# Performance work log

Hardware: AMD Instinct MI355X
Metric: run time of the kernel (lower is better)

The kernel has to match this reference:

```python
import jax, jax.numpy as jnp
import numpy as np

B, T, N = 16, 1024, 512

def setup_inputs() -> dict:
    key = jax.random.key(0)
    ks = jax.random.split(key, 6)
    scale = 1.0 / np.sqrt(N)
    x = jax.random.normal(ks[0], (B, T, N), dtype=jnp.float32)
    Wq = jax.random.normal(ks[1], (N, N), dtype=jnp.float32) * scale
    Wk = jax.random.normal(ks[2], (N, N), dtype=jnp.float32) * scale
    Wv = jax.random.normal(ks[3], (N, N), dtype=jnp.float32) * scale
    Wp = jax.random.normal(ks[4], (N, N), dtype=jnp.float32) * scale
    bp = jnp.zeros((N,), dtype=jnp.float32)
    return {"x": x, "Wq": Wq, "Wk": Wk, "Wv": Wv, "Wp": Wp, "bp": bp}

def reference(x, Wq, Wk, Wv, Wp, bp):
    # x: [B, T, N]; conv1d(k=1) over node channels == 'oi,bit->bot' on x^T [B,N,T]
    xt = jnp.swapaxes(x, -1, -2)                     # [B, N, T]
    q = jnp.einsum('oi,bit->bot', Wq, xt)            # [B, N, T]
    k = jnp.einsum('oi,bit->bot', Wk, xt)
    v = jnp.einsum('oi,bit->bot', Wv, xt)
    n = x.shape[-1]
    attn = jnp.einsum('bnt,bmt->bnm', q, k) * (n ** -0.5)  # [B, N, N]
    attn = jax.nn.softmax(attn, axis=-1)
    px = jnp.einsum('bnm,bmt->bnt', attn, v)         # [B, N, T]
    px = jnp.swapaxes(px, -1, -2)                    # [B, T, N]
    out = jnp.einsum('btn,on->bto', px, Wp) + bp     # Linear(N,N)
    return out
```

## Files before the change

### kernel.cpp

```cpp
#include <hip/hip_runtime.h>
#include <stdint.h>

#define BB 16
#define TT 1024
#define NN 512

typedef unsigned short u16;
typedef __bf16 bf16_t;
typedef bf16_t bf16x8 __attribute__((ext_vector_type(8)));
typedef float f32x4 __attribute__((ext_vector_type(4)));

struct alignas(8) U16x4 { u16 x, y, z, w; };
struct alignas(16) F32x4 { float x, y, z, w; };

__device__ __forceinline__ u16 f2bf(float f) {
    union { float f; uint32_t u; } v; v.f = f;
    uint32_t r = v.u + 0x7fffu + ((v.u >> 16) & 1u);
    return (u16)(r >> 16);
}

__device__ __forceinline__ void gload_lds16(const void* g, void* l) {
    __builtin_amdgcn_global_load_lds(
        (const __attribute__((address_space(1))) void*)g,
        (__attribute__((address_space(3))) void*)l, 16, 0, 0);
}

__device__ __forceinline__ void xcd_swizzle(int gx, int gy, int& bx, int& by) {
    const int nwg  = gx * gy;
    const int orig = by * gx + bx;
    const int q = nwg >> 3, r = nwg & 7;
    const int xcd = orig & 7, loc = orig >> 3;
    const int swz = (xcd < r ? xcd * (q + 1) : r * (q + 1) + (xcd - r) * q) + loc;
    bx = swz % gx;
    by = swz / gx;
}

__global__ __launch_bounds__(256)
void cvt_f32_bf16(const float* __restrict__ in, u16* __restrict__ out, int n4) {
    int i = blockIdx.x * blockDim.x + threadIdx.x;
    int stride = gridDim.x * blockDim.x;
    for (int c = i; c < n4; c += stride) {
        F32x4 f = ((const F32x4*)in)[c];
        U16x4 u;
        u.x = f2bf(f.x); u.y = f2bf(f.y); u.z = f2bf(f.z); u.w = f2bf(f.w);
        ((U16x4*)out)[c] = u;
    }
}

__global__ __launch_bounds__(256)
void cvt_weights(const float* __restrict__ Wq, const float* __restrict__ Wk,
                 const float* __restrict__ Wv, const float* __restrict__ Wp,
                 u16* __restrict__ out) {
    const int c = blockIdx.x * 256 + threadIdx.x;
    const int w = c >> 16;
    const int idx = c & 65535;
    const float* src = (w == 0) ? Wq : (w == 1) ? Wk : (w == 2) ? Wv : Wp;
    F32x4 f = ((const F32x4*)src)[idx];
    U16x4 u;
    u.x = f2bf(f.x); u.y = f2bf(f.y); u.z = f2bf(f.z); u.w = f2bf(f.w);
    ((U16x4*)out)[c] = u;
}

template<int MODE, int SPLITK>
__global__ __launch_bounds__(256)
void gemm_nt(const u16* __restrict__ Ag, const u16* __restrict__ Bg,
             void* __restrict__ Cg, const float* __restrict__ bias,
             int M, int Nc, int K, int lda, int ldb,
             long sA, long sB, long sC)
{
    int zb = blockIdx.z, kof = 0;
    if (SPLITK) { kof = (zb >> 4) * K; zb &= 15; }
    const u16* A  = Ag + (long)zb * sA + kof;
    const u16* Bt = Bg + (long)zb * sB + kof;

    __shared__ u16 As[8192];
    __shared__ u16 Bs[8192];

    int bx = blockIdx.x, by = blockIdx.y;
    xcd_swizzle(gridDim.x, gridDim.y, bx, by);

    const int tid  = threadIdx.x;
    const int wave = tid >> 6;
    const int lane = tid & 63;
    const int arow0 = by * 128;
    const int brow0 = bx * 128;
    const int wr = (wave >> 1) * 64;
    const int wc = (wave & 1) * 64;

    f32x4 zero = {0.f, 0.f, 0.f, 0.f};
    f32x4 acc[4][4];
#pragma unroll
    for (int i = 0; i < 4; i++)
#pragma unroll
        for (int j = 0; j < 4; j++) acc[i][j] = zero;

    const int kTiles = K >> 6;
    for (int kt = 0; kt < kTiles; ++kt) {
#pragma unroll
        for (int it = 0; it < 4; ++it) {
            const int off  = it * 4096 + wave * 1024 + lane * 16;
            const int row  = off >> 7;
            const int kb   = off & 127;
            const int gcol = kb ^ ((row & 7) << 4);
            gload_lds16((const char*)A  + ((long)(arow0 + row) * lda + kt * 64) * 2 + gcol,
                        (char*)As + it * 4096 + wave * 1024);
            gload_lds16((const char*)Bt + ((long)(brow0 + row) * ldb + kt * 64) * 2 + gcol,
                        (char*)Bs + it * 4096 + wave * 1024);
        }
        __syncthreads();

#pragma unroll
        for (int kk = 0; kk < 2; ++kk) {
            bf16x8 av[4], bv[4];
            const int kbyte = kk * 64 + ((lane >> 4) << 4);
#pragma unroll
            for (int m = 0; m < 4; m++) {
                const int row = wr + m * 16 + (lane & 15);
                av[m] = *(const bf16x8*)((const char*)As + row * 128 + (kbyte ^ ((row & 7) << 4)));
            }
#pragma unroll
            for (int n = 0; n < 4; n++) {
                const int row = wc + n * 16 + (lane & 15);
                bv[n] = *(const bf16x8*)((const char*)Bs + row * 128 + (kbyte ^ ((row & 7) << 4)));
            }
#pragma unroll
            for (int m = 0; m < 4; m++)
#pragma unroll
                for (int n = 0; n < 4; n++)
                    acc[m][n] = __builtin_amdgcn_mfma_f32_16x16x32_bf16(av[m], bv[n], acc[m][n], 0, 0, 0);
        }
        __syncthreads();
    }

    const int r0 = (lane >> 4) << 2;
    const int cl = lane & 15;
#pragma unroll
    for (int m = 0; m < 4; m++) {
        const long gm = (long)arow0 + wr + m * 16 + r0;
#pragma unroll
        for (int n = 0; n < 4; n++) {
            const long gn = (long)brow0 + wc + n * 16 + cl;
            if (MODE == 0) {
                u16* O = (u16*)Cg + blockIdx.z * sC;
#pragma unroll
                for (int r = 0; r < 4; r++)
                    O[(gm + r) * Nc + gn] = f2bf(acc[m][n][r]);
            } else if (MODE == 4) {
                const long b = gm >> 10;
                const long t = gm & 1023;
                if (gn < 1024) {
                    u16* O = (u16*)Cg + (gn >> 9) * ((long)BB * NN * TT);
                    const long col = gn & 511;
                    U16x4 u;
                    u.x = f2bf(acc[m][n][0]); u.y = f2bf(acc[m][n][1]);
                    u.z = f2bf(acc[m][n][2]); u.w = f2bf(acc[m][n][3]);
                    *(U16x4*)(O + (b * 512 + col) * 1024 + t) = u;
                } else {
                    u16* V = (u16*)Cg + 2L * BB * NN * TT;
                    const int vc = (int)gn - 1024;
#pragma unroll
                    for (int r = 0; r < 4; r++)
                        V[(gm + r) * NN + vc] = f2bf(acc[m][n][r]);
                }
            } else {
                float* O = (float*)Cg + blockIdx.z * sC;
                const float bb = (MODE == 3) ? bias[gn] : 0.f;
#pragma unroll
                for (int r = 0; r < 4; r++)
                    O[(gm + r) * Nc + gn] = acc[m][n][r] + bb;
            }
        }
    }
}

__global__ __launch_bounds__(256)
void softmax_rows(float* __restrict__ S0, const float* __restrict__ S1)
{
    const long r = blockIdx.x;
    float* row0 = S0 + r * 512;
    const float* row1 = S1 + r * 512;
    const int t = threadIdx.x;
    const int lane = t & 63, wave = t >> 6;
    const float scale = 0.04419417382415922f;

    float a = (row0[t]       + row1[t])       * scale;
    float b = (row0[t + 256] + row1[t + 256]) * scale;

    float m = fmaxf(a, b);
#pragma unroll
    for (int o = 32; o; o >>= 1) m = fmaxf(m, __shfl_xor(m, o, 64));

    __shared__ float red[8];
    if (lane == 0) red[wave] = m;
    __syncthreads();
    m = fmaxf(fmaxf(red[0], red[1]), fmaxf(red[2], red[3]));

    float e0 = __expf(a - m), e1 = __expf(b - m);
    float s = e0 + e1;
#pragma unroll
    for (int o = 32; o; o >>= 1) s += __shfl_xor(s, o, 64);
    if (lane == 0) red[wave + 4] = s;
    __syncthreads();
    s = red[4] + red[5] + red[6] + red[7];
    const float inv = 1.f / s;

    u16* P = (u16*)row0;
    P[t]       = f2bf(e0 * inv);
    P[t + 256] = f2bf(e1 * inv);
}

extern "C" void kernel_launch(void* const* d_in, const int* in_sizes, int n_in,
                              void* d_out, int out_size, void* d_ws, size_t ws_size,
                              hipStream_t stream)
{
    (void)in_sizes; (void)n_in; (void)out_size; (void)ws_size;
    const float* x  = (const float*)d_in[0];
    const float* Wq = (const float*)d_in[1];
    const float* Wk = (const float*)d_in[2];
    const float* Wv = (const float*)d_in[3];
    const float* Wp = (const float*)d_in[4];
    const float* bp = (const float*)d_in[5];
    float* out = (float*)d_out;

    char* ws = (char*)d_ws;
    size_t o = 0;
    auto alloc = [&](size_t bytes) {
        char* p = ws + o;
        o = (o + bytes + 255) & ~(size_t)255;
        return p;
    };
    u16* xb  = (u16*)alloc((size_t)BB * TT * NN * 2);
    u16* wb  = (u16*)alloc((size_t)4 * NN * NN * 2);
    u16* qkv = (u16*)alloc((size_t)3 * BB * NN * TT * 2);
    float* S = (float*)alloc((size_t)2 * BB * NN * NN * 4);
    u16* px  = xb;

    const u16* qb  = qkv;
    const u16* kbp = qkv + (size_t)BB * NN * TT;
    const u16* vb  = qkv + (size_t)2 * BB * NN * TT;
    const u16* wpb = wb + (size_t)3 * NN * NN;
    float* S1 = S + (size_t)BB * NN * NN;

    cvt_f32_bf16<<<dim3(2048), dim3(256), 0, stream>>>(x, xb, (BB * TT * NN) / 4);
    cvt_weights<<<dim3(1024), dim3(256), 0, stream>>>(Wq, Wk, Wv, Wp, wb);

    const dim3 blk(256);

    const dim3 gq(12, 128, 1);
    gemm_nt<4, 0><<<gq, blk, 0, stream>>>(xb, wb, qkv, nullptr,
                                          BB * TT, 1536, NN, NN, NN, 0, 0, 0);

    const dim3 g2(NN / 128, NN / 128, 2 * BB);
    gemm_nt<2, 1><<<g2, blk, 0, stream>>>(qb, kbp, S, nullptr, NN, NN, TT / 2, TT, TT,
                                          (long)NN * TT, (long)NN * TT, (long)NN * NN);

    softmax_rows<<<dim3(BB * NN), dim3(256), 0, stream>>>(S, S1);

    const dim3 g3(NN / 128, TT / 128, BB);
    gemm_nt<0, 0><<<g3, blk, 0, stream>>>(vb, (const u16*)S, px, nullptr, TT, NN, NN, NN, 1024,
                                          (long)TT * NN, (long)NN * 1024, (long)TT * NN);

    const dim3 g1(NN / 128, (BB * TT) / 128, 1);
    gemm_nt<3, 0><<<g1, blk, 0, stream>>>(px, wpb, out, bp, BB * TT, NN, NN, NN, NN, 0, 0, 0);
}
```

Before: 189.9 us.

## Double-buffer GEMM LDS tiles with BK=32 and merge conversion kernels

Rewrites the GEMM main loop to use two 32-wide K tiles in LDS. The next tile is prefetched with global_load_lds while MFMAs run on the current one, using manual vmcnt waits and raw s_barrier in place of __syncthreads. The LDS swizzle is adapted to the 64-byte row layout. It also fuses the x and weight fp32-to-bf16 conversion kernels into one launch with a flat grid. The smaller K tile doubles the barrier count per K, and the hand-written waitcnt logic carries correctness risk.

```diff
diff --git a/kernel.cpp b/kernel.cpp
--- a/kernel.cpp
+++ b/kernel.cpp
@@ -36,29 +36,29 @@
 }
 
 __global__ __launch_bounds__(256)
-void cvt_f32_bf16(const float* __restrict__ in, u16* __restrict__ out, int n4) {
-    int i = blockIdx.x * blockDim.x + threadIdx.x;
-    int stride = gridDim.x * blockDim.x;
-    for (int c = i; c < n4; c += stride) {
-        F32x4 f = ((const F32x4*)in)[c];
-        U16x4 u;
-        u.x = f2bf(f.x); u.y = f2bf(f.y); u.z = f2bf(f.z); u.w = f2bf(f.w);
-        ((U16x4*)out)[c] = u;
+void cvt_all(const float* __restrict__ x,
+             const float* __restrict__ Wq, const float* __restrict__ Wk,
+             const float* __restrict__ Wv, const float* __restrict__ Wp,
+             u16* __restrict__ xb, u16* __restrict__ wb) {
+    int c = blockIdx.x * 256 + threadIdx.x;
+    const float* src;
+    u16* dst;
+    int idx;
+    if (c < 2097152) {
+        src = x; dst = xb; idx = c;
+    } else {
+        c -= 2097152;
+        const int w = c >> 16;
+        idx = c & 65535;
+        src = (w == 0) ? Wq : (w == 1) ? Wk : (w == 2) ? Wv : Wp;
+        dst = wb + (w << 18);
+        idx += 0;
+        dst = wb; idx = (w << 16) + (c & 65535);
     }
-}
-
-__global__ __launch_bounds__(256)
-void cvt_weights(const float* __restrict__ Wq, const float* __restrict__ Wk,
-                 const float* __restrict__ Wv, const float* __restrict__ Wp,
-                 u16* __restrict__ out) {
-    const int c = blockIdx.x * 256 + threadIdx.x;
-    const int w = c >> 16;
-    const int idx = c & 65535;
-    const float* src = (w == 0) ? Wq : (w == 1) ? Wk : (w == 2) ? Wv : Wp;
-    F32x4 f = ((const F32x4*)src)[idx];
+    F32x4 f = ((const F32x4*)src)[ (src == x) ? idx : (idx & 65535) ];
     U16x4 u;
     u.x = f2bf(f.x); u.y = f2bf(f.y); u.z = f2bf(f.z); u.w = f2bf(f.w);
-    ((U16x4*)out)[c] = u;
+    ((U16x4*)dst)[idx] = u;
 }
 
 template<int MODE, int SPLITK>
@@ -73,8 +73,8 @@
     const u16* A  = Ag + (long)zb * sA + kof;
     const u16* Bt = Bg + (long)zb * sB + kof;
 
-    __shared__ u16 As[8192];
-    __shared__ u16 Bs[8192];
+    __shared__ u16 As[2][4096];
+    __shared__ u16 Bs[2][4096];
 
     int bx = blockIdx.x, by = blockIdx.y;
     xcd_swizzle(gridDim.x, gridDim.y, bx, by);
@@ -87,6 +87,14 @@
     const int wr = (wave >> 1) * 64;
     const int wc = (wave & 1) * 64;
 
+    const int srow  = tid >> 2;
+    const int sf    = ((srow >> 1) & 3) << 4;
+    const int gcol  = ((tid & 3) << 4) ^ sf;
+    const char* Asrc = (const char*)A  + (long)(arow0 + srow) * lda * 2 + gcol;
+    const char* Bsrc = (const char*)Bt + (long)(brow0 + srow) * ldb * 2 + gcol;
+    const long rstepA = (long)64 * lda * 2;
+    const long rstepB = (long)64 * ldb * 2;
+
     f32x4 zero = {0.f, 0.f, 0.f, 0.f};
     f32x4 acc[4][4];
 #pragma unroll
@@ -94,42 +102,55 @@
 #pragma unroll
         for (int j = 0; j < 4; j++) acc[i][j] = zero;
 
-    const int kTiles = K >> 6;
+    const int kTiles = K >> 5;
+
+    auto stage = [&](int buf, int kt) {
+        const long kb = (long)kt * 64;
+        char* ad = (char*)As + buf * 8192 + tid * 16;
+        char* bd = (char*)Bs + buf * 8192 + tid * 16;
+        gload_lds16(Asrc + kb,          ad);
+        gload_lds16(Bsrc + kb,          bd);
+        gload_lds16(Asrc + rstepA + kb, ad + 4096);
+        gload_lds16(Bsrc + rstepB + kb, bd + 4096);
+    };
+
+    stage(0, 0);
+    int cur = 0;
+    const int kbyte = (lane >> 4) << 4;
+    const int rA = lane & 15;
+
     for (int kt = 0; kt < kTiles; ++kt) {
-#pragma unroll
-        for (int it = 0; it < 4; ++it) {
-            const int off  = it * 4096 + wave * 1024 + lane * 16;
-            const int row  = off >> 7;
-            const int kb   = off & 127;
-            const int gcol = kb ^ ((row & 7) << 4);
-            gload_lds16((const char*)A  + ((long)(arow0 + row) * lda + kt * 64) * 2 + gcol,
-                        (char*)As + it * 4096 + wave * 1024);
-            gload_lds16((const char*)Bt + ((long)(brow0 + row) * ldb + kt * 64) * 2 + gcol,
-                        (char*)Bs + it * 4096 + wave * 1024);
-        }
-        __syncthreads();
-
-#pragma unroll
-        for (int kk = 0; kk < 2; ++kk) {
-            bf16x8 av[4], bv[4];
-            const int kbyte = kk * 64 + ((lane >> 4) << 4);
-#pragma unroll
-            for (int m = 0; m < 4; m++) {
-                const int row = wr + m * 16 + (lane & 15);
-                av[m] = *(const bf16x8*)((const char*)As + row * 128 + (kbyte ^ ((row & 7) << 4)));
-            }
-#pragma unroll
-            for (int n = 0; n < 4; n++) {
-                const int row = wc + n * 16 + (lane & 15);
-                bv[n] = *(const bf16x8*)((const char*)Bs + row * 128 + (kbyte ^ ((row & 7) << 4)));
-            }
-#pragma unroll
-            for (int m = 0; m < 4; m++)
-#pragma unroll
-                for (int n = 0; n < 4; n++)
-                    acc[m][n] = __builtin_amdgcn_mfma_f32_16x16x32_bf16(av[m], bv[n], acc[m][n], 0, 0, 0);
-        }
-        __syncthreads();
+        if (kt + 1 < kTiles) {
+            stage(cur ^ 1, kt + 1);
+            asm volatile("s_waitcnt vmcnt(4)" ::: "memory");
+        } else {
+            asm volatile("s_waitcnt vmcnt(0)" ::: "memory");
+        }
+        __builtin_amdgcn_s_barrier();
+        asm volatile("" ::: "memory");
+
+        bf16x8 av[4], bv[4];
+        const char* as = (const char*)As + cur * 8192;
+        const char* bs = (const char*)Bs + cur * 8192;
+#pragma unroll
+        for (int m = 0; m < 4; m++) {
+            const int row = wr + m * 16 + rA;
+            av[m] = *(const bf16x8*)(as + row * 64 + (kbyte ^ (((row >> 1) & 3) << 4)));
+        }
+#pragma unroll
+        for (int n = 0; n < 4; n++) {
+            const int row = wc + n * 16 + rA;
+            bv[n] = *(const bf16x8*)(bs + row * 64 + (kbyte ^ (((row >> 1) & 3) << 4)));
+        }
+#pragma unroll
+        for (int m = 0; m < 4; m++)
+#pragma unroll
+            for (int n = 0; n < 4; n++)
+                acc[m][n] = __builtin_amdgcn_mfma_f32_16x16x32_bf16(av[m], bv[n], acc[m][n], 0, 0, 0);
+
+        asm volatile("" ::: "memory");
+        __builtin_amdgcn_s_barrier();
+        cur ^= 1;
     }
 
     const int r0 = (lane >> 4) << 2;
@@ -241,8 +262,7 @@
     const u16* wpb = wb + (size_t)3 * NN * NN;
     float* S1 = S + (size_t)BB * NN * NN;
 
-    cvt_f32_bf16<<<dim3(2048), dim3(256), 0, stream>>>(x, xb, (BB * TT * NN) / 4);
-    cvt_weights<<<dim3(1024), dim3(256), 0, stream>>>(Wq, Wk, Wv, Wp, wb);
+    cvt_all<<<dim3(9216), dim3(256), 0, stream>>>(x, Wq, Wk, Wv, Wp, xb, wb);
 
     const dim3 blk(256);
 
```

Result: slower. 195.2 us (+2.8%).
